# Optimization experiments

Measured on AMD Instinct MI355X. Metric: run time of the kernel, lower is better.

The kernel has to match this reference:

```python
import jax, jax.numpy as jnp
import numpy as np

N = 100000      # nodes
D = 128         # input feature dim
K = 8           # propagation hops (concat K+1 blocks)
HID = 512
OUT = 32
E = 1600000     # edges (avg degree 16)
BN_EPS = 1e-5
DEG_EPS = 1e-8


def setup_inputs() -> dict:
    key = jax.random.key(0)
    ks = jax.random.split(key, 8)
    feature = jax.random.normal(ks[0], (N, D), dtype=jnp.float32)
    coor = jax.random.uniform(ks[1], (N, 2), dtype=jnp.float32)
    edge_index = jax.random.randint(ks[2], (2, E), 0, N, dtype=jnp.int32)
    theta = jnp.array(1.0, dtype=jnp.float32)  # Gaussian bandwidth param
    fan1 = D * (K + 1)
    W1 = jax.random.normal(ks[3], (HID, fan1), dtype=jnp.float32) * (1.0 / np.sqrt(fan1))
    b1 = jnp.zeros((HID,), dtype=jnp.float32)
    gamma = jnp.ones((HID,), dtype=jnp.float32)
    beta = jnp.zeros((HID,), dtype=jnp.float32)
    W2 = jax.random.normal(ks[4], (OUT, HID), dtype=jnp.float32) * (1.0 / np.sqrt(HID))
    b2 = jnp.zeros((OUT,), dtype=jnp.float32)
    return {"feature": feature, "coor": coor, "theta": theta,
            "W1": W1, "b1": b1, "gamma": gamma, "beta": beta,
            "W2": W2, "b2": b2, "edge_index": edge_index, "m": 1}


def reference(feature, coor, theta, W1, b1, gamma, beta, W2, b2, edge_index, m):
    row, col = edge_index[0], edge_index[1]  # dst, src
    # Gaussian kernel edge weights from coordinate distances (gather on coor)
    diff = coor[row] - coor[col]                       # [E, 2]
    dist2 = jnp.sum(diff * diff, axis=-1)              # [E]
    w = jnp.exp(-dist2 * theta / m)                    # [E]
    # degree (row) normalization via scatter-add
    deg = jax.ops.segment_sum(w, row, num_segments=N)  # [N]
    norm = w / (deg[row] + DEG_EPS)                    # [E]
    # K sequential propagations, concat with input (-> N x D*(K+1))
    xs = [feature]
    x = feature
    for _ in range(K):
        msgs = x[col] * norm[:, None]                  # [E, D] gather + weight
        x = jax.ops.segment_sum(msgs, row, num_segments=N)  # [N, D] scatter
        xs.append(x)
    h = jnp.concatenate(xs, axis=-1)                   # [N, D*(K+1)]
    # MLP head: fc1 -> leaky_relu(0.2) -> BatchNorm1d (batch stats) -> fc2
    h = jax.nn.leaky_relu(h @ W1.T + b1, negative_slope=0.2)
    mu = jnp.mean(h, axis=0)
    var = jnp.var(h, axis=0)
    h = (h - mu) * jax.lax.rsqrt(var + BN_EPS) * gamma + beta
    # dropout omitted (deterministic/eval reference)
    return h @ W2.T + b2
```

## Files before the change

kernel.cpp:

```cpp
#include <hip/hip_runtime.h>
#include <hip/hip_bf16.h>
#include <cstdint>
#include <cstddef>

#define NNODES 100000
#define DFEAT 128
#define KHOP 8
#define FAN1 1152
#define HIDN 512
#define OUTD 32
#define NEDGE 1600000
#define BN_EPS 1e-5f
#define DEG_EPS 1e-8f

using short8 = __attribute__((ext_vector_type(8))) short;
using f32x4  = __attribute__((ext_vector_type(4))) float;

__device__ __forceinline__ float bf16lo(uint32_t u) { return __uint_as_float(u << 16); }
__device__ __forceinline__ float bf16hi(uint32_t u) { return __uint_as_float(u & 0xffff0000u); }
__device__ __forceinline__ float bf16s(short x) {
    return __uint_as_float(((uint32_t)(uint16_t)x) << 16);
}
__device__ __forceinline__ uint32_t packbf(float a, float b) {
    uint32_t lo = __bfloat16_as_ushort(__float2bfloat16(a));
    uint32_t hi = __bfloat16_as_ushort(__float2bfloat16(b));
    return lo | (hi << 16);
}

__device__ __forceinline__ void gload16(const void* g, void* l) {
    __builtin_amdgcn_global_load_lds(
        (const __attribute__((address_space(1))) uint32_t*)g,
        (__attribute__((address_space(3))) uint32_t*)l, 16, 0, 0);
}

struct Blk9 { const __hip_bfloat16* p[9]; };

__global__ __launch_bounds__(256) void edge_kernel(
    const int* __restrict__ ei, const float* __restrict__ coor,
    const float* __restrict__ theta, const int* __restrict__ mm,
    float* __restrict__ deg, int* __restrict__ cnt)
{
    int e = blockIdx.x * 256 + threadIdx.x;
    if (e >= NEDGE) return;
    float tom = theta[0] / (float)mm[0];
    int r = ei[e], c = ei[NEDGE + e];
    float2 pr = *(const float2*)(coor + 2*(size_t)r);
    float2 pc = *(const float2*)(coor + 2*(size_t)c);
    float dx = pr.x - pc.x, dy = pr.y - pc.y;
    float w = expf(-(dx*dx + dy*dy) * tom);
    atomicAdd(&deg[r], w);
    atomicAdd(&cnt[r], 1);
}

__global__ __launch_bounds__(1024) void scan_local(
    const int* __restrict__ cnt, int* __restrict__ row_ptr,
    int* __restrict__ bsum, int n)
{
    __shared__ int wsum[16];
    int b = blockIdx.x, tid = threadIdx.x;
    int i = b * 1024 + tid;
    int lane = tid & 63, wv = tid >> 6;
    int v = (i < n) ? cnt[i] : 0;
    #pragma unroll
    for (int off = 1; off < 64; off <<= 1) {
        int t = __shfl_up(v, off, 64);
        if (lane >= off) v += t;
    }
    if (lane == 63) wsum[wv] = v;
    __syncthreads();
    if (tid < 16) {
        int t = wsum[tid];
        #pragma unroll
        for (int off = 1; off < 16; off <<= 1) {
            int u = __shfl_up(t, off, 64);
            if (tid >= off) t += u;
        }
        wsum[tid] = t;
    }
    __syncthreads();
    int incl = v + ((wv == 0) ? 0 : wsum[wv - 1]);
    if (i < n) row_ptr[i + 1] = incl;
    if (tid == 0) bsum[b] = wsum[15];
}

__global__ __launch_bounds__(128) void scan_carry(int* __restrict__ bsum, int n)
{
    __shared__ int ws[2];
    int tid = threadIdx.x, lane = tid & 63, wv = tid >> 6;
    int v = (tid < n) ? bsum[tid] : 0;
    int incl = v;
    #pragma unroll
    for (int off = 1; off < 64; off <<= 1) {
        int t = __shfl_up(incl, off, 64);
        if (lane >= off) incl += t;
    }
    if (lane == 63) ws[wv] = incl;
    __syncthreads();
    int excl = incl - v + ((wv == 0) ? 0 : ws[0]);
    if (tid < n) bsum[tid] = excl;
}

__global__ __launch_bounds__(256) void scan_add(
    const int* __restrict__ bsum, int* __restrict__ row_ptr, int n)
{
    int i = blockIdx.x * 256 + threadIdx.x;
    if (i == 0) row_ptr[0] = 0;
    if (i < n) row_ptr[i + 1] += bsum[i >> 10];
}

__global__ __launch_bounds__(256) void fill_kernel(
    const int* __restrict__ ei, const float* __restrict__ coor,
    const float* __restrict__ theta, const int* __restrict__ mm,
    const float* __restrict__ deg, const int* __restrict__ row_ptr,
    int* __restrict__ fill, int* __restrict__ cols, float* __restrict__ nrm)
{
    int e = blockIdx.x * 256 + threadIdx.x;
    if (e >= NEDGE) return;
    float tom = theta[0] / (float)mm[0];
    int r = ei[e], c = ei[NEDGE + e];
    float2 pr = *(const float2*)(coor + 2*(size_t)r);
    float2 pc = *(const float2*)(coor + 2*(size_t)c);
    float dx = pr.x - pc.x, dy = pr.y - pc.y;
    float w = expf(-(dx*dx + dy*dy) * tom);
    int pos = row_ptr[r] + atomicAdd(&fill[r], 1);
    cols[pos] = c;
    nrm[pos] = w / (deg[r] + DEG_EPS);
}

__global__ __launch_bounds__(256) void cast_feat_kernel(
    const float* __restrict__ f, __hip_bfloat16* __restrict__ x0)
{
    int i = blockIdx.x * 256 + threadIdx.x;
    int node = i >> 6, l2 = i & 63;
    if (node >= NNODES) return;
    float2 v = *(const float2*)(f + (size_t)node * DFEAT + l2 * 2);
    __hip_bfloat162 hb;
    hb.x = __float2bfloat16(v.x);
    hb.y = __float2bfloat16(v.y);
    *(__hip_bfloat162*)(x0 + (size_t)node * DFEAT + l2 * 2) = hb;
}

__global__ __launch_bounds__(256) void cast_w1_kernel(
    const float* __restrict__ w1, __hip_bfloat16* __restrict__ o)
{
    int i = blockIdx.x * 256 + threadIdx.x;
    if (i < HIDN * FAN1) o[i] = __float2bfloat16(w1[i]);
}

__global__ __launch_bounds__(256) void prop_kernel(
    const __hip_bfloat16* __restrict__ x, __hip_bfloat16* __restrict__ y,
    const int* __restrict__ row_ptr, const int* __restrict__ cols,
    const float* __restrict__ nrm)
{
    int gw = (blockIdx.x * 256 + threadIdx.x) >> 6;
    if (gw >= NNODES) return;
    int lane = threadIdx.x & 63;
    int q = lane >> 4, sl = lane & 15;
    int beg = row_ptr[gw], end = row_ptr[gw + 1];
    float a0 = 0.f, a1 = 0.f, a2 = 0.f, a3 = 0.f;
    float a4 = 0.f, a5 = 0.f, a6 = 0.f, a7 = 0.f;
    int e = beg + q;
    for (; e + 12 < end; e += 16) {
        int s0 = cols[e], s1 = cols[e + 4], s2 = cols[e + 8], s3 = cols[e + 12];
        float w0 = nrm[e], w1 = nrm[e + 4], w2 = nrm[e + 8], w3 = nrm[e + 12];
        uint4 u0 = *(const uint4*)(x + (size_t)s0 * DFEAT + sl * 8);
        uint4 u1 = *(const uint4*)(x + (size_t)s1 * DFEAT + sl * 8);
        uint4 u2 = *(const uint4*)(x + (size_t)s2 * DFEAT + sl * 8);
        uint4 u3 = *(const uint4*)(x + (size_t)s3 * DFEAT + sl * 8);
        a0 += w0 * bf16lo(u0.x); a1 += w0 * bf16hi(u0.x);
        a2 += w0 * bf16lo(u0.y); a3 += w0 * bf16hi(u0.y);
        a4 += w0 * bf16lo(u0.z); a5 += w0 * bf16hi(u0.z);
        a6 += w0 * bf16lo(u0.w); a7 += w0 * bf16hi(u0.w);
        a0 += w1 * bf16lo(u1.x); a1 += w1 * bf16hi(u1.x);
        a2 += w1 * bf16lo(u1.y); a3 += w1 * bf16hi(u1.y);
        a4 += w1 * bf16lo(u1.z); a5 += w1 * bf16hi(u1.z);
        a6 += w1 * bf16lo(u1.w); a7 += w1 * bf16hi(u1.w);
        a0 += w2 * bf16lo(u2.x); a1 += w2 * bf16hi(u2.x);
        a2 += w2 * bf16lo(u2.y); a3 += w2 * bf16hi(u2.y);
        a4 += w2 * bf16lo(u2.z); a5 += w2 * bf16hi(u2.z);
        a6 += w2 * bf16lo(u2.w); a7 += w2 * bf16hi(u2.w);
        a0 += w3 * bf16lo(u3.x); a1 += w3 * bf16hi(u3.x);
        a2 += w3 * bf16lo(u3.y); a3 += w3 * bf16hi(u3.y);
        a4 += w3 * bf16lo(u3.z); a5 += w3 * bf16hi(u3.z);
        a6 += w3 * bf16lo(u3.w); a7 += w3 * bf16hi(u3.w);
    }
    for (; e < end; e += 4) {
        int s0 = cols[e];
        float w0 = nrm[e];
        uint4 u0 = *(const uint4*)(x + (size_t)s0 * DFEAT + sl * 8);
        a0 += w0 * bf16lo(u0.x); a1 += w0 * bf16hi(u0.x);
        a2 += w0 * bf16lo(u0.y); a3 += w0 * bf16hi(u0.y);
        a4 += w0 * bf16lo(u0.z); a5 += w0 * bf16hi(u0.z);
        a6 += w0 * bf16lo(u0.w); a7 += w0 * bf16hi(u0.w);
    }
    a0 += __shfl_xor(a0, 16, 64); a0 += __shfl_xor(a0, 32, 64);
    a1 += __shfl_xor(a1, 16, 64); a1 += __shfl_xor(a1, 32, 64);
    a2 += __shfl_xor(a2, 16, 64); a2 += __shfl_xor(a2, 32, 64);
    a3 += __shfl_xor(a3, 16, 64); a3 += __shfl_xor(a3, 32, 64);
    a4 += __shfl_xor(a4, 16, 64); a4 += __shfl_xor(a4, 32, 64);
    a5 += __shfl_xor(a5, 16, 64); a5 += __shfl_xor(a5, 32, 64);
    a6 += __shfl_xor(a6, 16, 64); a6 += __shfl_xor(a6, 32, 64);
    a7 += __shfl_xor(a7, 16, 64); a7 += __shfl_xor(a7, 32, 64);
    if (q == 0) {
        uint4 o;
        o.x = packbf(a0, a1);
        o.y = packbf(a2, a3);
        o.z = packbf(a4, a5);
        o.w = packbf(a6, a7);
        *(uint4*)(y + (size_t)gw * DFEAT + sl * 8) = o;
    }
}

__global__ __launch_bounds__(256) void fc1_kernel(
    Blk9 blks, const __hip_bfloat16* __restrict__ w1,
    const float* __restrict__ b1, __hip_bfloat16* __restrict__ h1,
    float* __restrict__ gsum, float* __restrict__ gsq,
    int nblk, int kb0, int mode)
{
    __shared__ char smem[33792];
    char* As = smem;
    char* Bs = smem + 16384;

    int n0 = blockIdx.x * 128;
    int m0 = blockIdx.y * 128;
    int tid = threadIdx.x, lane = tid & 63, wv = tid >> 6;
    int wr = wv >> 1, wc = wv & 1;

    f32x4 acc[4][4];
    #pragma unroll
    for (int i = 0; i < 4; ++i)
        #pragma unroll
        for (int j = 0; j < 4; ++j)
            acc[i][j] = (f32x4){0.f, 0.f, 0.f, 0.f};

    for (int kb = 0; kb < nblk; ++kb) {
        const __hip_bfloat16* xp = blks.p[kb];
        int kglob = (kb0 + kb) * 128;
        #pragma unroll
        for (int half = 0; half < 2; ++half) {
            int koff = half * 64;
            __syncthreads();
            #pragma unroll
            for (int l = 0; l < 4; ++l) {
                int u = l * 256 + wv * 64 + lane;
                int row = u >> 3;
                int ch = (u & 7) ^ (row & 7);
                gload16(xp + (size_t)(m0 + row) * DFEAT + koff + ch * 8,
                        As + (l * 256 + wv * 64) * 16);
                gload16(w1 + (size_t)(n0 + row) * FAN1 + kglob + koff + ch * 8,
                        Bs + (l * 256 + wv * 64) * 16);
            }
            __syncthreads();
            #pragma unroll
            for (int ks = 0; ks < 2; ++ks) {
                short8 af[4], bfr[4];
                #pragma unroll
                for (int i = 0; i < 4; ++i) {
                    int row = wr * 64 + i * 16 + (lane & 15);
                    int ch = (ks * 4 + (lane >> 4)) ^ (row & 7);
                    af[i] = *(const short8*)(As + row * 128 + ch * 16);
                }
                #pragma unroll
                for (int j = 0; j < 4; ++j) {
                    int row = wc * 64 + j * 16 + (lane & 15);
                    int ch = (ks * 4 + (lane >> 4)) ^ (row & 7);
                    bfr[j] = *(const short8*)(Bs + row * 128 + ch * 16);
                }
                #pragma unroll
                for (int j = 0; j < 4; ++j)
                    #pragma unroll
                    for (int i = 0; i < 4; ++i)
                        acc[i][j] = __builtin_amdgcn_mfma_f32_16x16x32_bf16(af[i], bfr[j], acc[i][j], 0, 0, 0);
            }
        }
    }

    __syncthreads();
    __hip_bfloat16* tile = (__hip_bfloat16*)smem;
    float* lsum = (float*)(smem + 32768);
    float* lsq  = lsum + 128;
    bool fin = (mode & 2) != 0;
    if (fin && tid < 128) { lsum[tid] = 0.f; lsq[tid] = 0.f; }
    #pragma unroll
    for (int i = 0; i < 4; ++i) {
        #pragma unroll
        for (int j = 0; j < 4; ++j) {
            int col = wc * 64 + j * 16 + (lane & 15);
            #pragma unroll
            for (int r = 0; r < 4; ++r) {
                int row = wr * 64 + i * 16 + (lane >> 4) * 4 + r;
                tile[row * 128 + col] = __float2bfloat16(acc[i][j][r]);
            }
        }
    }
    __syncthreads();

    int cu = tid & 15, tr = tid >> 4;
    float bias[8];
    float s[8], q[8];
    #pragma unroll
    for (int e = 0; e < 8; ++e) { s[e] = 0.f; q[e] = 0.f; }
    if (fin) {
        #pragma unroll
        for (int e = 0; e < 8; ++e) bias[e] = b1[n0 + cu * 8 + e];
    }
    for (int p = 0; p < 8; ++p) {
        int row = p * 16 + tr;
        int gm = m0 + row;
        if (gm >= NNODES) continue;
        short8 fresh = *(const short8*)(tile + row * 128 + cu * 8);
        size_t gidx = (size_t)gm * HIDN + n0 + cu * 8;
        float v[8];
        #pragma unroll
        for (int e = 0; e < 8; ++e) v[e] = bf16s(fresh[e]);
        if (mode & 1) {
            short8 prev = *(const short8*)(h1 + gidx);
            #pragma unroll
            for (int e = 0; e < 8; ++e) v[e] += bf16s(prev[e]);
        }
        if (fin) {
            #pragma unroll
            for (int e = 0; e < 8; ++e) {
                float t = v[e] + bias[e];
                t = (t > 0.f) ? t : 0.2f * t;
                v[e] = t;
                s[e] += t;
                q[e] += t * t;
            }
        }
        short8 outv;
        #pragma unroll
        for (int e = 0; e < 8; ++e) outv[e] = (short)__bfloat16_as_ushort(__float2bfloat16(v[e]));
        *(short8*)(h1 + gidx) = outv;
    }
    if (fin) {
        #pragma unroll
        for (int e = 0; e < 8; ++e) {
            atomicAdd(&lsum[cu * 8 + e], s[e]);
            atomicAdd(&lsq[cu * 8 + e], q[e]);
        }
        __syncthreads();
        if (tid < 128) {
            atomicAdd(&gsum[n0 + tid], lsum[tid]);
            atomicAdd(&gsq[n0 + tid], lsq[tid]);
        }
    }
}

__global__ __launch_bounds__(512) void bn_finalize(
    const float* __restrict__ gsum, const float* __restrict__ gsq,
    const float* __restrict__ gamma, const float* __restrict__ beta,
    const float* __restrict__ w2, const float* __restrict__ b2,
    __hip_bfloat16* __restrict__ w2s, float* __restrict__ cvec)
{
    __shared__ float ts[HIDN];
    int tid = threadIdx.x;
    float mu = gsum[tid] * (1.0f / NNODES);
    float var = gsq[tid] * (1.0f / NNODES) - mu * mu;
    float s = gamma[tid] * rsqrtf(var + BN_EPS);
    float t = beta[tid] - mu * s;
    ts[tid] = t;
    for (int o = 0; o < OUTD; ++o)
        w2s[o * HIDN + tid] = __float2bfloat16(w2[o * HIDN + tid] * s);
    __syncthreads();
    int lane = tid & 63, wv = tid >> 6;
    for (int o = wv; o < OUTD; o += 8) {
        float p = 0.f;
        for (int j = lane; j < HIDN; j += 64) p += ts[j] * w2[o * HIDN + j];
        #pragma unroll
        for (int off = 32; off; off >>= 1) p += __shfl_xor(p, off, 64);
        if (lane == 0) cvec[o] = p + b2[o];
    }
}

__global__ __launch_bounds__(256) void fc2_kernel(
    const __hip_bfloat16* __restrict__ h1, const __hip_bfloat16* __restrict__ w2s,
    const float* __restrict__ cvec, float* __restrict__ out)
{
    int gw = (blockIdx.x * 256 + threadIdx.x) >> 6;
    if (gw >= NNODES / 16) return;
    int lane = threadIdx.x & 63;
    int m0 = gw * 16;
    f32x4 acc[2];
    acc[0] = (f32x4){0.f, 0.f, 0.f, 0.f};
    acc[1] = (f32x4){0.f, 0.f, 0.f, 0.f};
    #pragma unroll
    for (int kt = 0; kt < HIDN / 32; ++kt) {
        int k0 = kt * 32;
        short8 a = *(const short8*)(h1 + (size_t)(m0 + (lane & 15)) * HIDN + k0 + (lane >> 4) * 8);
        #pragma unroll
        for (int j = 0; j < 2; ++j) {
            short8 b = *(const short8*)(w2s + (size_t)(j * 16 + (lane & 15)) * HIDN + k0 + (lane >> 4) * 8);
            acc[j] = __builtin_amdgcn_mfma_f32_16x16x32_bf16(a, b, acc[j], 0, 0, 0);
        }
    }
    #pragma unroll
    for (int j = 0; j < 2; ++j) {
        int col = j * 16 + (lane & 15);
        float cadd = cvec[col];
        #pragma unroll
        for (int r = 0; r < 4; ++r) {
            int row = m0 + (lane >> 4) * 4 + r;
            out[(size_t)row * OUTD + col] = acc[j][r] + cadd;
        }
    }
}

struct Ptrs {
    float *deg, *nrm, *gsum, *gsq, *cvec;
    int *cnt, *fillc, *row_ptr, *colsb, *bsum;
    __hip_bfloat16 *slot[9], *h1acc, *w1b, *w2s;
};

static size_t layout(char* base, int nslots, Ptrs& P) {
    char* p = base;
    auto take = [&](size_t b) {
        char* q = (char*)(((uintptr_t)p + 255) & ~(uintptr_t)255);
        p = q + b;
        return q;
    };
    P.deg     = (float*)take((size_t)NNODES * 4);
    P.cnt     = (int*)  take((size_t)NNODES * 4);
    P.fillc   = (int*)  take((size_t)NNODES * 4);
    P.row_ptr = (int*)  take((size_t)(NNODES + 1) * 4);
    P.bsum    = (int*)  take(128 * 4);
    P.colsb   = (int*)  take((size_t)NEDGE * 4);
    P.nrm     = (float*)take((size_t)NEDGE * 4);
    P.h1acc   = (__hip_bfloat16*)take((size_t)NNODES * HIDN * 2);
    P.w1b     = (__hip_bfloat16*)take((size_t)HIDN * FAN1 * 2);
    P.w2s     = (__hip_bfloat16*)take((size_t)OUTD * HIDN * 2);
    P.gsum    = (float*)take(HIDN * 4);
    P.gsq     = (float*)take(HIDN * 4);
    P.cvec    = (float*)take(OUTD * 4);
    for (int i = 0; i < 9; ++i) P.slot[i] = nullptr;
    for (int i = 0; i < nslots; ++i)
        P.slot[i] = (__hip_bfloat16*)take((size_t)NNODES * DFEAT * 2 + 32768);
    return (size_t)(p - base);
}

extern "C" void kernel_launch(void* const* d_in, const int* in_sizes, int n_in,
                              void* d_out, int out_size, void* d_ws, size_t ws_size,
                              hipStream_t stream)
{
    const float* feature = (const float*)d_in[0];
    const float* coor    = (const float*)d_in[1];
    const float* theta   = (const float*)d_in[2];
    const float* W1      = (const float*)d_in[3];
    const float* b1      = (const float*)d_in[4];
    const float* gamma   = (const float*)d_in[5];
    const float* beta    = (const float*)d_in[6];
    const float* W2      = (const float*)d_in[7];
    const float* b2      = (const float*)d_in[8];
    const int*   ei      = (const int*)d_in[9];
    const int*   mm      = (const int*)d_in[10];
    float* out = (float*)d_out;
    (void)in_sizes; (void)n_in; (void)out_size;

    Ptrs P;
    size_t need9 = layout((char*)0, 9, P);
    size_t need5 = layout((char*)0, 5, P);
    int nslots = (ws_size >= need9) ? 9 : (ws_size >= need5) ? 5 : 3;
    layout((char*)d_ws, nslots, P);

    hipMemsetAsync(P.deg,   0, (size_t)NNODES * 4, stream);
    hipMemsetAsync(P.cnt,   0, (size_t)NNODES * 4, stream);
    hipMemsetAsync(P.fillc, 0, (size_t)NNODES * 4, stream);
    hipMemsetAsync(P.gsum,  0, HIDN * 4, stream);
    hipMemsetAsync(P.gsq,   0, HIDN * 4, stream);

    int eb = (NEDGE + 255) / 256;
    int nchunk = (NNODES + 1023) / 1024;
    edge_kernel<<<eb, 256, 0, stream>>>(ei, coor, theta, mm, P.deg, P.cnt);
    scan_local<<<nchunk, 1024, 0, stream>>>(P.cnt, P.row_ptr, P.bsum, NNODES);
    scan_carry<<<1, 128, 0, stream>>>(P.bsum, nchunk);
    scan_add<<<(NNODES + 255) / 256, 256, 0, stream>>>(P.bsum, P.row_ptr, NNODES);
    fill_kernel<<<eb, 256, 0, stream>>>(ei, coor, theta, mm, P.deg, P.row_ptr,
                                        P.fillc, P.colsb, P.nrm);

    cast_w1_kernel<<<(HIDN * FAN1 + 255) / 256, 256, 0, stream>>>(W1, P.w1b);
    cast_feat_kernel<<<(NNODES * 64) / 256, 256, 0, stream>>>(feature, P.slot[0]);

    int pb = (NNODES * 64) / 256;
    dim3 fgrid(4, (NNODES + 127) / 128);

    auto launch_fc1 = [&](int first_slot, int nblk, int kb0, int mode) {
        Blk9 b;
        for (int i = 0; i < 9; ++i) b.p[i] = P.slot[0];
        for (int i = 0; i < nblk; ++i) b.p[i] = P.slot[(first_slot + i) % nslots];
        fc1_kernel<<<fgrid, 256, 0, stream>>>(b, P.w1b, b1, P.h1acc,
                                              P.gsum, P.gsq, nblk, kb0, mode);
    };

    for (int k = 1; k <= KHOP; ++k) {
        prop_kernel<<<pb, 256, 0, stream>>>(P.slot[(k - 1) % nslots],
                                            P.slot[k % nslots],
                                            P.row_ptr, P.colsb, P.nrm);
        if (nslots == 5 && k == 4) launch_fc1(0, 5, 0, 0);
        if (nslots == 3 && k == 2) launch_fc1(0, 3, 0, 0);
        if (nslots == 3 && k == 5) launch_fc1(0, 3, 3, 1);
    }
    if (nslots == 9) launch_fc1(0, 9, 0, 2);
    if (nslots == 5) launch_fc1(0, 4, 5, 3);
    if (nslots == 3) launch_fc1(0, 3, 6, 3);

    bn_finalize<<<1, 512, 0, stream>>>(P.gsum, P.gsq, gamma, beta, W2, b2,
                                       P.w2s, P.cvec);
    fc2_kernel<<<(NNODES / 16 * 64 + 255) / 256, 256, 0, stream>>>(P.h1acc, P.w2s,
                                                                   P.cvec, out);
}
```

Baseline: 1.059 ms.

## Double-buffer fc1 LDS tiles with K=32 stages and remap block ids

Rewrites the fc1 GEMM main loop to use two LDS buffers with 32-wide K stages, prefetching the next stage via async global-to-LDS loads while MFMAs consume the current one, with a vmcnt wait replacing full syncthreads pairs. It also flattens the grid to 1D and remaps block ids so that blocks landing on the same XCD share neighbouring row tiles, aiming for better L2 reuse of activations. The XOR swizzle is removed, so LDS reads may suffer more bank conflicts. The grid size of 8*391 covers 3128 tiles against 3128 needed, so it relies on exact tile count.

```diff
diff --git a/kernel.cpp b/kernel.cpp
--- a/kernel.cpp
+++ b/kernel.cpp
@@ -218,11 +218,10 @@
     int nblk, int kb0, int mode)
 {
     __shared__ char smem[33792];
-    char* As = smem;
-    char* Bs = smem + 16384;
-
-    int n0 = blockIdx.x * 128;
-    int m0 = blockIdx.y * 128;
+    int pid = blockIdx.x;
+    int lid = (pid & 7) * 391 + (pid >> 3);
+    int n0 = (lid & 3) * 128;
+    int m0 = (lid >> 2) * 128;
     int tid = threadIdx.x, lane = tid & 63, wv = tid >> 6;
     int wr = wv >> 1, wc = wv & 1;
 
@@ -233,47 +232,52 @@
         for (int j = 0; j < 4; ++j)
             acc[i][j] = (f32x4){0.f, 0.f, 0.f, 0.f};
 
-    for (int kb = 0; kb < nblk; ++kb) {
-        const __hip_bfloat16* xp = blks.p[kb];
-        int kglob = (kb0 + kb) * 128;
-        #pragma unroll
-        for (int half = 0; half < 2; ++half) {
-            int koff = half * 64;
-            __syncthreads();
+    int nkt = nblk * 4;
+
+#define STAGE(hb, ktv) do {                                                   \
+        const __hip_bfloat16* xp = blks.p[(ktv) >> 2];                        \
+        int koff_ = ((ktv) & 3) * 32;                                         \
+        int kglob_ = (kb0 + ((ktv) >> 2)) * 128 + koff_;                      \
+        char* Ab_ = smem + (hb) * 16384;                                      \
+        char* Bb_ = Ab_ + 8192;                                               \
+        _Pragma("unroll")                                                     \
+        for (int l = 0; l < 2; ++l) {                                         \
+            int u = l * 256 + wv * 64 + lane;                                 \
+            int row_ = u >> 2, qq_ = u & 3;                                   \
+            gload16(xp + (size_t)(m0 + row_) * DFEAT + koff_ + qq_ * 8,       \
+                    Ab_ + u * 16);                                            \
+            gload16(w1 + (size_t)(n0 + row_) * FAN1 + kglob_ + qq_ * 8,       \
+                    Bb_ + u * 16);                                            \
+        }                                                                     \
+    } while (0)
+
+    STAGE(0, 0);
+    for (int kt = 0; kt < nkt; ++kt) {
+        int cur = kt & 1;
+        __builtin_amdgcn_s_barrier();
+        if (kt + 1 < nkt) {
+            STAGE(cur ^ 1, kt + 1);
+            asm volatile("s_waitcnt vmcnt(4)" ::: "memory");
+        } else {
+            asm volatile("s_waitcnt vmcnt(0)" ::: "memory");
+        }
+        __builtin_amdgcn_s_barrier();
+        char* Ab = smem + cur * 16384;
+        char* Bb = Ab + 8192;
+        short8 af[4], bfr[4];
+        #pragma unroll
+        for (int i = 0; i < 4; ++i)
+            af[i] = *(const short8*)(Ab + (wr * 64 + i * 16 + (lane & 15)) * 64 + (lane >> 4) * 16);
+        #pragma unroll
+        for (int j = 0; j < 4; ++j)
+            bfr[j] = *(const short8*)(Bb + (wc * 64 + j * 16 + (lane & 15)) * 64 + (lane >> 4) * 16);
+        #pragma unroll
+        for (int j = 0; j < 4; ++j)
             #pragma unroll
-            for (int l = 0; l < 4; ++l) {
-                int u = l * 256 + wv * 64 + lane;
-                int row = u >> 3;
-                int ch = (u & 7) ^ (row & 7);
-                gload16(xp + (size_t)(m0 + row) * DFEAT + koff + ch * 8,
-                        As + (l * 256 + wv * 64) * 16);
-                gload16(w1 + (size_t)(n0 + row) * FAN1 + kglob + koff + ch * 8,
-                        Bs + (l * 256 + wv * 64) * 16);
-            }
-            __syncthreads();
-            #pragma unroll
-            for (int ks = 0; ks < 2; ++ks) {
-                short8 af[4], bfr[4];
-                #pragma unroll
-                for (int i = 0; i < 4; ++i) {
-                    int row = wr * 64 + i * 16 + (lane & 15);
-                    int ch = (ks * 4 + (lane >> 4)) ^ (row & 7);
-                    af[i] = *(const short8*)(As + row * 128 + ch * 16);
-                }
-                #pragma unroll
-                for (int j = 0; j < 4; ++j) {
-                    int row = wc * 64 + j * 16 + (lane & 15);
-                    int ch = (ks * 4 + (lane >> 4)) ^ (row & 7);
-                    bfr[j] = *(const short8*)(Bs + row * 128 + ch * 16);
-                }
-                #pragma unroll
-                for (int j = 0; j < 4; ++j)
-                    #pragma unroll
-                    for (int i = 0; i < 4; ++i)
-                        acc[i][j] = __builtin_amdgcn_mfma_f32_16x16x32_bf16(af[i], bfr[j], acc[i][j], 0, 0, 0);
-            }
-        }
-    }
+            for (int i = 0; i < 4; ++i)
+                acc[i][j] = __builtin_amdgcn_mfma_f32_16x16x32_bf16(af[i], bfr[j], acc[i][j], 0, 0, 0);
+    }
+#undef STAGE
 
     __syncthreads();
     __hip_bfloat16* tile = (__hip_bfloat16*)smem;
@@ -481,7 +485,7 @@
     cast_feat_kernel<<<(NNODES * 64) / 256, 256, 0, stream>>>(feature, P.slot[0]);
 
     int pb = (NNODES * 64) / 256;
-    dim3 fgrid(4, (NNODES + 127) / 128);
+    int fgrid = 8 * 391;
 
     auto launch_fc1 = [&](int first_slot, int nblk, int kb0, int mode) {
         Blk9 b;
```

New measurement: 1.012 ms. 4.4% less time.

## Restructure fc1 GEMM to stream A from registers with fixed three-slot schedule

Applied to the files above, without the earlier changes.

The fc1 GEMM is reworked so each block computes a 256x64 tile. Only the W1 slice is staged in padded LDS; the activation fragments are loaded straight from global memory into registers with double buffering. A swizzled 1D block index groups the 8 column tiles of a row band to improve L2 reuse of activations. The workspace now always uses three rotating slots with three fc1 launches, dropping the 9- and 5-slot variants, which means extra read-modify-write passes over h1 when more workspace was available.

```diff
diff --git a/kernel.cpp b/kernel.cpp
--- a/kernel.cpp
+++ b/kernel.cpp
@@ -27,13 +27,7 @@
     return lo | (hi << 16);
 }
 
-__device__ __forceinline__ void gload16(const void* g, void* l) {
-    __builtin_amdgcn_global_load_lds(
-        (const __attribute__((address_space(1))) uint32_t*)g,
-        (__attribute__((address_space(3))) uint32_t*)l, 16, 0, 0);
-}
-
-struct Blk9 { const __hip_bfloat16* p[9]; };
+struct Blk3 { const __hip_bfloat16* p[3]; };
 
 __global__ __launch_bounds__(256) void edge_kernel(
     const int* __restrict__ ei, const float* __restrict__ coor,
@@ -211,20 +205,22 @@
     }
 }
 
+#define BROW 400
 __global__ __launch_bounds__(256) void fc1_kernel(
-    Blk9 blks, const __hip_bfloat16* __restrict__ w1,
+    Blk3 blks, const __hip_bfloat16* __restrict__ w1,
     const float* __restrict__ b1, __hip_bfloat16* __restrict__ h1,
     float* __restrict__ gsum, float* __restrict__ gsq,
-    int nblk, int kb0, int mode)
-{
-    __shared__ char smem[33792];
-    char* As = smem;
-    char* Bs = smem + 16384;
-
-    int n0 = blockIdx.x * 128;
-    int m0 = blockIdx.y * 128;
+    int kb0, int mode)
+{
+    __shared__ char smem[26112];
+    int pid = blockIdx.x;
+    int lid = (pid & 7) * 391 + (pid >> 3);
+    int mt = lid >> 3, nt = lid & 7;
+    int m0 = mt * 256, n0 = nt * 64;
     int tid = threadIdx.x, lane = tid & 63, wv = tid >> 6;
-    int wr = wv >> 1, wc = wv & 1;
+    int mw = m0 + wv * 64;
+    int arow = mw + (lane & 15);
+    int kcol = (lane >> 4) * 8;
 
     f32x4 acc[4][4];
     #pragma unroll
@@ -233,114 +229,128 @@
         for (int j = 0; j < 4; ++j)
             acc[i][j] = (f32x4){0.f, 0.f, 0.f, 0.f};
 
-    for (int kb = 0; kb < nblk; ++kb) {
-        const __hip_bfloat16* xp = blks.p[kb];
-        int kglob = (kb0 + kb) * 128;
-        #pragma unroll
-        for (int half = 0; half < 2; ++half) {
-            int koff = half * 64;
-            __syncthreads();
+    short8 afA[4], afB[4];
+
+#define LOADAF(dst, ktv) do {                                                  \
+        const __hip_bfloat16* xp_ = blks.p[(ktv) >> 2];                        \
+        int ko_ = ((ktv) & 3) * 32 + kcol;                                     \
+        _Pragma("unroll")                                                      \
+        for (int i_ = 0; i_ < 4; ++i_)                                         \
+            dst[i_] = *(const short8*)(xp_ + (size_t)(arow + i_ * 16) * DFEAT + ko_); \
+    } while (0)
+
+#define MFMA16(src, tloc) do {                                                 \
+        _Pragma("unroll")                                                      \
+        for (int j_ = 0; j_ < 4; ++j_) {                                       \
+            short8 bfr_ = *(const short8*)(smem +                              \
+                (j_ * 16 + (lane & 15)) * BROW + (tloc) * 64 + kcol * 2);      \
+            _Pragma("unroll")                                                  \
+            for (int i_ = 0; i_ < 4; ++i_)                                     \
+                acc[i_][j_] = __builtin_amdgcn_mfma_f32_16x16x32_bf16(         \
+                    src[i_], bfr_, acc[i_][j_], 0, 0, 0);                      \
+        }                                                                      \
+    } while (0)
+
+    #pragma unroll
+    for (int ph = 0; ph < 2; ++ph) {
+        __syncthreads();
+        int kglob0 = kb0 * 128 + ph * 192;
+        #pragma unroll
+        for (int i = 0; i < 6; ++i) {
+            int c = i * 256 + tid;
+            int nn = c / 24, kc = c - nn * 24;
+            short8 v = *(const short8*)(w1 + (size_t)(n0 + nn) * FAN1 + kglob0 + kc * 8);
+            *(short8*)(smem + nn * BROW + kc * 16) = v;
+        }
+        __syncthreads();
+
+        LOADAF(afA, ph * 6 + 0);
+        #pragma unroll
+        for (int tp = 0; tp < 3; ++tp) {
+            int t0 = tp * 2;
+            LOADAF(afB, ph * 6 + t0 + 1);
+            MFMA16(afA, t0);
+            if (t0 + 2 < 6) LOADAF(afA, ph * 6 + t0 + 2);
+            MFMA16(afB, t0 + 1);
+        }
+    }
+#undef LOADAF
+#undef MFMA16
+
+    __syncthreads();
+    __hip_bfloat16* tile = (__hip_bfloat16*)smem;
+    float* lsum = (float*)(smem + 16384);
+    float* lsq  = lsum + 64;
+    bool fin = (mode & 2) != 0;
+    if (fin && tid < 64) { lsum[tid] = 0.f; lsq[tid] = 0.f; }
+
+    int ck = tid & 7, tr = tid >> 3;
+    float bias[8];
+    float s[8], q[8];
+    #pragma unroll
+    for (int e = 0; e < 8; ++e) { s[e] = 0.f; q[e] = 0.f; }
+    if (fin) {
+        #pragma unroll
+        for (int e = 0; e < 8; ++e) bias[e] = b1[n0 + ck * 8 + e];
+    }
+
+    #pragma unroll
+    for (int hh = 0; hh < 2; ++hh) {
+        __syncthreads();
+        if ((wv >> 1) == hh) {
             #pragma unroll
-            for (int l = 0; l < 4; ++l) {
-                int u = l * 256 + wv * 64 + lane;
-                int row = u >> 3;
-                int ch = (u & 7) ^ (row & 7);
-                gload16(xp + (size_t)(m0 + row) * DFEAT + koff + ch * 8,
-                        As + (l * 256 + wv * 64) * 16);
-                gload16(w1 + (size_t)(n0 + row) * FAN1 + kglob + koff + ch * 8,
-                        Bs + (l * 256 + wv * 64) * 16);
-            }
-            __syncthreads();
-            #pragma unroll
-            for (int ks = 0; ks < 2; ++ks) {
-                short8 af[4], bfr[4];
-                #pragma unroll
-                for (int i = 0; i < 4; ++i) {
-                    int row = wr * 64 + i * 16 + (lane & 15);
-                    int ch = (ks * 4 + (lane >> 4)) ^ (row & 7);
-                    af[i] = *(const short8*)(As + row * 128 + ch * 16);
-                }
+            for (int i = 0; i < 4; ++i) {
                 #pragma unroll
                 for (int j = 0; j < 4; ++j) {
-                    int row = wc * 64 + j * 16 + (lane & 15);
-                    int ch = (ks * 4 + (lane >> 4)) ^ (row & 7);
-                    bfr[j] = *(const short8*)(Bs + row * 128 + ch * 16);
+                    int col = j * 16 + (lane & 15);
+                    #pragma unroll
+                    for (int r = 0; r < 4; ++r) {
+                        int row = (wv & 1) * 64 + i * 16 + (lane >> 4) * 4 + r;
+                        tile[row * 64 + col] = __float2bfloat16(acc[i][j][r]);
+                    }
                 }
+            }
+        }
+        __syncthreads();
+        #pragma unroll
+        for (int p = 0; p < 4; ++p) {
+            int row = p * 32 + tr;
+            int gm = m0 + hh * 128 + row;
+            if (gm >= NNODES) continue;
+            short8 fresh = *(const short8*)(tile + row * 64 + ck * 8);
+            size_t gidx = (size_t)gm * HIDN + n0 + ck * 8;
+            float v[8];
+            #pragma unroll
+            for (int e = 0; e < 8; ++e) v[e] = bf16s(fresh[e]);
+            if (mode & 1) {
+                short8 prev = *(const short8*)(h1 + gidx);
                 #pragma unroll
-                for (int j = 0; j < 4; ++j)
-                    #pragma unroll
-                    for (int i = 0; i < 4; ++i)
-                        acc[i][j] = __builtin_amdgcn_mfma_f32_16x16x32_bf16(af[i], bfr[j], acc[i][j], 0, 0, 0);
+                for (int e = 0; e < 8; ++e) v[e] += bf16s(prev[e]);
             }
-        }
-    }
-
-    __syncthreads();
-    __hip_bfloat16* tile = (__hip_bfloat16*)smem;
-    float* lsum = (float*)(smem + 32768);
-    float* lsq  = lsum + 128;
-    bool fin = (mode & 2) != 0;
-    if (fin && tid < 128) { lsum[tid] = 0.f; lsq[tid] = 0.f; }
-    #pragma unroll
-    for (int i = 0; i < 4; ++i) {
-        #pragma unroll
-        for (int j = 0; j < 4; ++j) {
-            int col = wc * 64 + j * 16 + (lane & 15);
+            if (fin) {
+                #pragma unroll
+                for (int e = 0; e < 8; ++e) {
+                    float t = v[e] + bias[e];
+                    t = (t > 0.f) ? t : 0.2f * t;
+                    v[e] = t;
+                    s[e] += t;
+                    q[e] += t * t;
+                }
+            }
+            short8 outv;
             #pragma unroll
-            for (int r = 0; r < 4; ++r) {
-                int row = wr * 64 + i * 16 + (lane >> 4) * 4 + r;
-                tile[row * 128 + col] = __float2bfloat16(acc[i][j][r]);
-            }
-        }
-    }
-    __syncthreads();
-
-    int cu = tid & 15, tr = tid >> 4;
-    float bias[8];
-    float s[8], q[8];
-    #pragma unroll
-    for (int e = 0; e < 8; ++e) { s[e] = 0.f; q[e] = 0.f; }
+            for (int e = 0; e < 8; ++e) outv[e] = (short)__bfloat16_as_ushort(__float2bfloat16(v[e]));
+            *(short8*)(h1 + gidx) = outv;
+        }
+    }
     if (fin) {
         #pragma unroll
-        for (int e = 0; e < 8; ++e) bias[e] = b1[n0 + cu * 8 + e];
-    }
-    for (int p = 0; p < 8; ++p) {
-        int row = p * 16 + tr;
-        int gm = m0 + row;
-        if (gm >= NNODES) continue;
-        short8 fresh = *(const short8*)(tile + row * 128 + cu * 8);
-        size_t gidx = (size_t)gm * HIDN + n0 + cu * 8;
-        float v[8];
-        #pragma unroll
-        for (int e = 0; e < 8; ++e) v[e] = bf16s(fresh[e]);
-        if (mode & 1) {
-            short8 prev = *(const short8*)(h1 + gidx);
-            #pragma unroll
-            for (int e = 0; e < 8; ++e) v[e] += bf16s(prev[e]);
-        }
-        if (fin) {
-            #pragma unroll
-            for (int e = 0; e < 8; ++e) {
-                float t = v[e] + bias[e];
-                t = (t > 0.f) ? t : 0.2f * t;
-                v[e] = t;
-                s[e] += t;
-                q[e] += t * t;
-            }
-        }
-        short8 outv;
-        #pragma unroll
-        for (int e = 0; e < 8; ++e) outv[e] = (short)__bfloat16_as_ushort(__float2bfloat16(v[e]));
-        *(short8*)(h1 + gidx) = outv;
-    }
-    if (fin) {
-        #pragma unroll
         for (int e = 0; e < 8; ++e) {
-            atomicAdd(&lsum[cu * 8 + e], s[e]);
-            atomicAdd(&lsq[cu * 8 + e], q[e]);
+            atomicAdd(&lsum[ck * 8 + e], s[e]);
+            atomicAdd(&lsq[ck * 8 + e], q[e]);
         }
         __syncthreads();
-        if (tid < 128) {
+        if (tid < 64) {
             atomicAdd(&gsum[n0 + tid], lsum[tid]);
             atomicAdd(&gsq[n0 + tid], lsq[tid]);
         }
@@ -409,10 +419,10 @@
 struct Ptrs {
     float *deg, *nrm, *gsum, *gsq, *cvec;
     int *cnt, *fillc, *row_ptr, *colsb, *bsum;
-    __hip_bfloat16 *slot[9], *h1acc, *w1b, *w2s;
+    __hip_bfloat16 *slot[3], *h1acc, *w1b, *w2s;
 };
 
-static size_t layout(char* base, int nslots, Ptrs& P) {
+static size_t layout(char* base, Ptrs& P) {
     char* p = base;
     auto take = [&](size_t b) {
         char* q = (char*)(((uintptr_t)p + 255) & ~(uintptr_t)255);
@@ -432,9 +442,8 @@
     P.gsum    = (float*)take(HIDN * 4);
     P.gsq     = (float*)take(HIDN * 4);
     P.cvec    = (float*)take(OUTD * 4);
-    for (int i = 0; i < 9; ++i) P.slot[i] = nullptr;
-    for (int i = 0; i < nslots; ++i)
-        P.slot[i] = (__hip_bfloat16*)take((size_t)NNODES * DFEAT * 2 + 32768);
+    for (int i = 0; i < 3; ++i)
+        P.slot[i] = (__hip_bfloat16*)take((size_t)NNODES * DFEAT * 2 + 65536);
     return (size_t)(p - base);
 }
 
@@ -454,13 +463,10 @@
     const int*   ei      = (const int*)d_in[9];
     const int*   mm      = (const int*)d_in[10];
     float* out = (float*)d_out;
-    (void)in_sizes; (void)n_in; (void)out_size;
+    (void)in_sizes; (void)n_in; (void)out_size; (void)ws_size;
 
     Ptrs P;
-    size_t need9 = layout((char*)0, 9, P);
-    size_t need5 = layout((char*)0, 5, P);
-    int nslots = (ws_size >= need9) ? 9 : (ws_size >= need5) ? 5 : 3;
-    layout((char*)d_ws, nslots, P);
+    layout((char*)d_ws, P);
 
     hipMemsetAsync(P.deg,   0, (size_t)NNODES * 4, stream);
     hipMemsetAsync(P.cnt,   0, (size_t)NNODES * 4, stream);
@@ -481,27 +487,23 @@
     cast_feat_kernel<<<(NNODES * 64) / 256, 256, 0, stream>>>(feature, P.slot[0]);
 
     int pb = (NNODES * 64) / 256;
-    dim3 fgrid(4, (NNODES + 127) / 128);
-
-    auto launch_fc1 = [&](int first_slot, int nblk, int kb0, int mode) {
-        Blk9 b;
-        for (int i = 0; i < 9; ++i) b.p[i] = P.slot[0];
-        for (int i = 0; i < nblk; ++i) b.p[i] = P.slot[(first_slot + i) % nslots];
+    int fgrid = 8 * 391;
+
+    auto launch_fc1 = [&](int kb0, int mode) {
+        Blk3 b;
+        for (int i = 0; i < 3; ++i) b.p[i] = P.slot[i];
         fc1_kernel<<<fgrid, 256, 0, stream>>>(b, P.w1b, b1, P.h1acc,
-                                              P.gsum, P.gsq, nblk, kb0, mode);
+                                              P.gsum, P.gsq, kb0, mode);
     };
 
     for (int k = 1; k <= KHOP; ++k) {
-        prop_kernel<<<pb, 256, 0, stream>>>(P.slot[(k - 1) % nslots],
-                                            P.slot[k % nslots],
+        prop_kernel<<<pb, 256, 0, stream>>>(P.slot[(k - 1) % 3],
+                                            P.slot[k % 3],
                                             P.row_ptr, P.colsb, P.nrm);
-        if (nslots == 5 && k == 4) launch_fc1(0, 5, 0, 0);
-        if (nslots == 3 && k == 2) launch_fc1(0, 3, 0, 0);
-        if (nslots == 3 && k == 5) launch_fc1(0, 3, 3, 1);
-    }
-    if (nslots == 9) launch_fc1(0, 9, 0, 2);
-    if (nslots == 5) launch_fc1(0, 4, 5, 3);
-    if (nslots == 3) launch_fc1(0, 3, 6, 3);
+        if (k == 2) launch_fc1(0, 0);
+        if (k == 5) launch_fc1(3, 1);
+    }
+    launch_fc1(6, 3);
 
     bn_finalize<<<1, 512, 0, stream>>>(P.gsum, P.gsq, gamma, beta, W2, b2,
                                        P.w2s, P.cvec);
```

Measured after the change: 1.141 ms. +7.8%, slower.
